# Kernel optimization log

Measured on AMD Instinct MI355X. Metric: run time of the kernel, lower is better.

The kernel has to match this reference:

```python
import jax, jax.numpy as jnp
import numpy as np

N, F_IN, D_OUT, H = 8192, 512, 64, 8
ALPHA = 0.2
NEG_INF = jnp.float32(-9e15)


def setup_inputs() -> dict:
    key = jax.random.key(0)
    k1, k2, k3, k4, k5 = jax.random.split(key, 5)
    x = jax.random.normal(k1, (N, F_IN), dtype=jnp.float32)
    # sparse-ish binary adjacency (avg degree ~33) with self-loops, stored dense
    adj = (jax.random.uniform(k2, (N, N)) < 0.004).astype(jnp.float32)
    adj = jnp.maximum(adj, jnp.eye(N, dtype=jnp.float32))
    W = jax.random.normal(k3, (H, F_IN, D_OUT), dtype=jnp.float32) * 0.05
    a1 = jax.random.normal(k4, (H, D_OUT), dtype=jnp.float32) * 0.05
    a2 = jax.random.normal(k5, (H, D_OUT), dtype=jnp.float32) * 0.05
    return {"x": x, "adj": adj, "W": W, "a1": a1, "a2": a2}


def reference(x, adj, W, a1, a2):
    mask = adj > 0
    outputs = []
    for h in range(H):  # fixed small head count (matches original per-head loop)
        Wh = x @ W[h]                      # [N, D]
        f1 = Wh @ a1[h]                    # [N]
        f2 = Wh @ a2[h]                    # [N]
        e = jax.nn.leaky_relu(f1[:, None] + f2[None, :], ALPHA)  # [N, N]
        att = jnp.where(mask, e, NEG_INF)
        att = jax.nn.softmax(att, axis=1)  # dropout omitted (eval mode)
        outputs.append(att @ Wh)           # [N, D]
    return jnp.concatenate(outputs, axis=1)  # [N, H*D]
```

## Files before the change

kernel.cpp:

```cpp
#include <hip/hip_runtime.h>
#include <hip/hip_bf16.h>
#include <cstdint>

#define N_NODES 8192
#define F_IN    512
#define D_O     64
#define H_N     8
#define NOUT    512
#define MAXD    128

#define BM 64
#define BN 128
#define BK 64

typedef __attribute__((ext_vector_type(8))) short short8;
typedef __attribute__((ext_vector_type(4))) float f32x4;

static __device__ __forceinline__ ushort f2bf(float f) {
  union { float f; uint32_t u; } v; v.f = f;
  uint32_t r = v.u + 0x7FFFu + ((v.u >> 16) & 1u);
  return (ushort)(r >> 16);
}
static __device__ __forceinline__ float bf2f(ushort u) {
  union { uint32_t u; float f; } v; v.u = ((uint32_t)u) << 16;
  return v.f;
}

__global__ __launch_bounds__(256) void convert(const float* __restrict__ x,
                                               const float* __restrict__ W,
                                               ushort* __restrict__ xb,
                                               ushort* __restrict__ Wt) {
  __shared__ float Ws[64][65];
  const int b = blockIdx.x, t = threadIdx.x;
  if (b < 2048) {
    const int gid = b * 256 + t;
    #pragma unroll
    for (int it = 0; it < 2; ++it) {
      const int q = gid + it * 524288;
      const float4 v = ((const float4*)x)[q];
      ushort4 u;
      u.x = f2bf(v.x); u.y = f2bf(v.y); u.z = f2bf(v.z); u.w = f2bf(v.w);
      ((ushort4*)xb)[q] = u;
    }
  } else {
    const int bb = b - 2048;
    const int h = bb >> 3, kt = bb & 7;
    const int d = t & 63, krg = (t >> 6) * 16;
    const float* src = &W[((size_t)h * F_IN + kt * 64 + krg) * D_O + d];
    #pragma unroll
    for (int q = 0; q < 16; ++q)
      Ws[krg + q][d] = src[(size_t)q * D_O];
    __syncthreads();
    const int d0 = t >> 2, kq = (t & 3) * 16;
    ushort* dst = &Wt[(size_t)h * D_O * F_IN + (size_t)d0 * F_IN + kt * 64 + kq];
    #pragma unroll
    for (int q = 0; q < 16; ++q)
      dst[q] = f2bf(Ws[kq + q][d0]);
  }
}

__global__ __launch_bounds__(256) void scan_gemm(const uint32_t* __restrict__ adj,
                                                 const ushort* __restrict__ xb,
                                                 const ushort* __restrict__ Wt,
                                                 const float* __restrict__ a1,
                                                 const float* __restrict__ a2,
                                                 ushort* __restrict__ Whb,
                                                 float* __restrict__ f1,
                                                 float* __restrict__ f2,
                                                 ushort* __restrict__ nbr_g,
                                                 int* __restrict__ deg_g) {
  __shared__ ushort As[BM][BK + 8];
  __shared__ ushort Bs[BN][BK + 8];
  __shared__ int wsum[4];

  const int id   = blockIdx.x;
  const int tid  = threadIdx.x;
  const int lane = tid & 63;
  const int wv   = tid >> 6;

  if (id < 512) {
    const int wr = wv >> 1, wc = wv & 1;
    const int r0 = (id >> 2) * BM;
    const int c0 = (id & 3) * BN;
    const int lm = lane & 15;
    const int lg = lane >> 4;

    f32x4 acc[2][4];
    #pragma unroll
    for (int m2 = 0; m2 < 2; ++m2)
      #pragma unroll
      for (int n2 = 0; n2 < 4; ++n2)
        acc[m2][n2] = (f32x4){0.f, 0.f, 0.f, 0.f};

    for (int k0 = 0; k0 < F_IN; k0 += BK) {
      __syncthreads();
      #pragma unroll
      for (int p = 0; p < 2; ++p) {
        const int e = p * 256 + tid;
        const int row = e >> 3, ck = (e & 7) * 8;
        *(short8*)&As[row][ck] = *(const short8*)&xb[(size_t)(r0 + row) * F_IN + k0 + ck];
      }
      #pragma unroll
      for (int p = 0; p < 4; ++p) {
        const int e = p * 256 + tid;
        const int row = e >> 3, ck = (e & 7) * 8;
        *(short8*)&Bs[row][ck] = *(const short8*)&Wt[(size_t)(c0 + row) * F_IN + k0 + ck];
      }
      __syncthreads();

      #pragma unroll
      for (int kk = 0; kk < 2; ++kk) {
        const int koff = kk * 32 + lg * 8;
        short8 af[2], bf[4];
        #pragma unroll
        for (int m2 = 0; m2 < 2; ++m2)
          af[m2] = *(const short8*)&As[wr * 32 + m2 * 16 + lm][koff];
        #pragma unroll
        for (int n2 = 0; n2 < 4; ++n2)
          bf[n2] = *(const short8*)&Bs[wc * 64 + n2 * 16 + lm][koff];
        #pragma unroll
        for (int m2 = 0; m2 < 2; ++m2)
          #pragma unroll
          for (int n2 = 0; n2 < 4; ++n2)
            acc[m2][n2] = __builtin_amdgcn_mfma_f32_16x16x32_bf16(af[m2], bf[n2], acc[m2][n2], 0, 0, 0);
      }
    }

    const int head = (c0 >> 6) + wc;
    float a1v[4], a2v[4];
    #pragma unroll
    for (int n2 = 0; n2 < 4; ++n2) {
      a1v[n2] = a1[head * D_O + n2 * 16 + lm];
      a2v[n2] = a2[head * D_O + n2 * 16 + lm];
    }
    #pragma unroll
    for (int m2 = 0; m2 < 2; ++m2) {
      #pragma unroll
      for (int r = 0; r < 4; ++r) {
        const int row = r0 + wr * 32 + m2 * 16 + lg * 4 + r;
        float p1 = 0.f, p2 = 0.f;
        #pragma unroll
        for (int n2 = 0; n2 < 4; ++n2) {
          const float v = acc[m2][n2][r];
          p1 += v * a1v[n2];
          p2 += v * a2v[n2];
          Whb[(size_t)row * NOUT + c0 + wc * 64 + n2 * 16 + lm] = f2bf(v);
        }
        #pragma unroll
        for (int o = 1; o < 16; o <<= 1) {
          p1 += __shfl_xor(p1, o);
          p2 += __shfl_xor(p2, o);
        }
        if (lm == 0) {
          f1[(size_t)row * H_N + head] = p1;
          f2[(size_t)row * H_N + head] = p2;
        }
      }
    }
  } else {
    const int i = id - 512;
    const uint32_t* arow = adj + (size_t)i * N_NODES;
    uint32_t bits = 0;
    #pragma unroll
    for (int u = 0; u < 8; ++u) {
      const uint4 a = *(const uint4*)&arow[(u * 256 + tid) * 4];
      if (a.x) bits |= 1u << (u * 4 + 0);
      if (a.y) bits |= 1u << (u * 4 + 1);
      if (a.z) bits |= 1u << (u * 4 + 2);
      if (a.w) bits |= 1u << (u * 4 + 3);
    }
    const int cnt = __popc(bits);
    int v = cnt;
    #pragma unroll
    for (int o = 1; o < 64; o <<= 1) {
      int u = __shfl_up(v, o);
      if (lane >= o) v += u;
    }
    if (lane == 63) wsum[wv] = v;
    __syncthreads();
    int base = 0, total = 0;
    #pragma unroll
    for (int ww = 0; ww < 4; ++ww) {
      int s = wsum[ww];
      if (ww < wv) base += s;
      total += s;
    }
    int off = base + v - cnt;
    #pragma unroll
    for (int u = 0; u < 8; ++u)
      #pragma unroll
      for (int bq = 0; bq < 4; ++bq)
        if (bits & (1u << (u * 4 + bq))) {
          if (off < MAXD) nbr_g[(size_t)i * MAXD + off] = (ushort)((u * 256 + tid) * 4 + bq);
          ++off;
        }
    if (tid == 0) deg_g[i] = min(total, MAXD);
  }
}

__global__ __launch_bounds__(64) void gat_panel(const ushort* __restrict__ nbr_g,
                                                const int* __restrict__ deg_g,
                                                const ushort* __restrict__ Whb,
                                                const float* __restrict__ f1,
                                                const float* __restrict__ f2,
                                                float* __restrict__ out) {
  const int bid = blockIdx.x;
  const int xcd = bid & 7;
  const int P   = xcd >> 1;
  const int i   = (bid >> 3) * 2 + (xcd & 1);
  const int t   = threadIdx.x;

  __shared__ int   nbr[MAXD];
  __shared__ float ff[MAXD][2];
  __shared__ float ps[MAXD][2];
  __shared__ float f1s2[2], invs2[2];

  const int deg = deg_g[i];
  nbr[t]      = nbr_g[(size_t)i * MAXD + t];
  nbr[t + 64] = nbr_g[(size_t)i * MAXD + t + 64];
  if (t < 2) f1s2[t] = f1[(size_t)i * H_N + 2 * P + t];
  __syncthreads();

  for (int n = t; n < deg; n += 64) {
    const float2 v = *(const float2*)&f2[(size_t)nbr[n] * H_N + 2 * P];
    ff[n][0] = v.x; ff[n][1] = v.y;
  }
  __syncthreads();

  {
    const int h = t >> 5;
    const int l = t & 31;
    const float f1v = f1s2[h];
    float m = -3.0e38f;
    for (int n = l; n < deg; n += 32) {
      float e = f1v + ff[n][h];
      e = e > 0.f ? e : 0.2f * e;
      ps[n][h] = e;
      m = fmaxf(m, e);
    }
    #pragma unroll
    for (int o = 16; o; o >>= 1) m = fmaxf(m, __shfl_xor(m, o));
    float s = 0.f;
    for (int n = l; n < deg; n += 32) {
      const float e = __expf(ps[n][h] - m);
      ps[n][h] = e;
      s += e;
    }
    #pragma unroll
    for (int o = 16; o; o >>= 1) s += __shfl_xor(s, o);
    if (l == 0) invs2[h] = 1.0f / s;
  }
  __syncthreads();

  const int ht      = t >> 5;
  const int colbase = P * 128 + t * 2;
  float a0 = 0.f, a1c = 0.f;
  #pragma unroll 8
  for (int n = 0; n < deg; ++n) {
    const float pv = ps[n][ht];
    const ushort2 u = *(const ushort2*)&Whb[(size_t)nbr[n] * NOUT + colbase];
    a0  += pv * bf2f(u.x);
    a1c += pv * bf2f(u.y);
  }
  const float inv = invs2[ht];
  float2 o2; o2.x = a0 * inv; o2.y = a1c * inv;
  *(float2*)&out[(size_t)i * NOUT + colbase] = o2;
}

extern "C" void kernel_launch(void* const* d_in, const int* in_sizes, int n_in,
                              void* d_out, int out_size, void* d_ws, size_t ws_size,
                              hipStream_t stream) {
  const float* x   = (const float*)d_in[0];
  const float* adj = (const float*)d_in[1];
  const float* W   = (const float*)d_in[2];
  const float* a1  = (const float*)d_in[3];
  const float* a2  = (const float*)d_in[4];
  float* out = (float*)d_out;

  ushort* Whb = (ushort*)d_ws;
  ushort* xb  = Whb + (size_t)N_NODES * NOUT;
  ushort* Wt  = xb + (size_t)N_NODES * F_IN;
  float*  f1  = (float*)(Wt + (size_t)H_N * D_O * F_IN);
  float*  f2  = f1 + (size_t)N_NODES * H_N;
  ushort* nbr_g = (ushort*)(f2 + (size_t)N_NODES * H_N);
  int*    deg_g = (int*)(nbr_g + (size_t)N_NODES * MAXD);

  hipLaunchKernelGGL(convert, dim3(2112), dim3(256), 0, stream, x, W, xb, Wt);
  hipLaunchKernelGGL(scan_gemm, dim3(512 + N_NODES), dim3(256), 0, stream,
                     (const uint32_t*)adj, xb, Wt, a1, a2, Whb, f1, f2, nbr_g, deg_g);
  hipLaunchKernelGGL(gat_panel, dim3(4 * N_NODES), dim3(64), 0, stream,
                     nbr_g, deg_g, Whb, f1, f2, out);
}
```

Before: 92.26 us.

## Pack four rows per block in gat_panel and drop block barriers

```diff
diff --git a/kernel.cpp b/kernel.cpp
--- a/kernel.cpp
+++ b/kernel.cpp
@@ -198,71 +198,51 @@
   }
 }
 
-__global__ __launch_bounds__(64) void gat_panel(const ushort* __restrict__ nbr_g,
-                                                const int* __restrict__ deg_g,
-                                                const ushort* __restrict__ Whb,
-                                                const float* __restrict__ f1,
-                                                const float* __restrict__ f2,
-                                                float* __restrict__ out) {
+__global__ __launch_bounds__(256) void gat_panel(const ushort* __restrict__ nbr_g,
+                                                 const int* __restrict__ deg_g,
+                                                 const ushort* __restrict__ Whb,
+                                                 const float* __restrict__ f1,
+                                                 const float* __restrict__ f2,
+                                                 float* __restrict__ out) {
   const int bid = blockIdx.x;
   const int xcd = bid & 7;
   const int P   = xcd >> 1;
-  const int i   = (bid >> 3) * 2 + (xcd & 1);
-  const int t   = threadIdx.x;
-
-  __shared__ int   nbr[MAXD];
-  __shared__ float ff[MAXD][2];
-  __shared__ float ps[MAXD][2];
-  __shared__ float f1s2[2], invs2[2];
+  const int w   = threadIdx.x >> 6;
+  const int i   = (bid >> 3) * 8 + (xcd & 1) * 4 + w;
+  const int t   = threadIdx.x & 63;
+
+  __shared__ int   nbr[4][MAXD];
+  __shared__ float ps[4][MAXD][2];
 
   const int deg = deg_g[i];
-  nbr[t]      = nbr_g[(size_t)i * MAXD + t];
-  nbr[t + 64] = nbr_g[(size_t)i * MAXD + t + 64];
-  if (t < 2) f1s2[t] = f1[(size_t)i * H_N + 2 * P + t];
-  __syncthreads();
-
-  for (int n = t; n < deg; n += 64) {
-    const float2 v = *(const float2*)&f2[(size_t)nbr[n] * H_N + 2 * P];
-    ff[n][0] = v.x; ff[n][1] = v.y;
-  }
-  __syncthreads();
-
-  {
-    const int h = t >> 5;
-    const int l = t & 31;
-    const float f1v = f1s2[h];
-    float m = -3.0e38f;
-    for (int n = l; n < deg; n += 32) {
-      float e = f1v + ff[n][h];
-      e = e > 0.f ? e : 0.2f * e;
-      ps[n][h] = e;
-      m = fmaxf(m, e);
-    }
-    #pragma unroll
-    for (int o = 16; o; o >>= 1) m = fmaxf(m, __shfl_xor(m, o));
-    float s = 0.f;
-    for (int n = l; n < deg; n += 32) {
-      const float e = __expf(ps[n][h] - m);
-      ps[n][h] = e;
-      s += e;
-    }
-    #pragma unroll
-    for (int o = 16; o; o >>= 1) s += __shfl_xor(s, o);
-    if (l == 0) invs2[h] = 1.0f / s;
-  }
-  __syncthreads();
-
-  const int ht      = t >> 5;
+  if (t < deg)      nbr[w][t]      = nbr_g[(size_t)i * MAXD + t];
+  if (t + 64 < deg) nbr[w][t + 64] = nbr_g[(size_t)i * MAXD + t + 64];
+
+  const int h = t >> 5;
+  const int l = t & 31;
+  const float f1v = f1[(size_t)i * H_N + 2 * P + h];
+  float s = 0.f;
+  for (int n = l; n < deg; n += 32) {
+    const float2 v = *(const float2*)&f2[(size_t)nbr[w][n] * H_N + 2 * P];
+    float e = f1v + (h ? v.y : v.x);
+    e = e > 0.f ? e : 0.2f * e;
+    e = __expf(e);
+    ps[w][n][h] = e;
+    s += e;
+  }
+  #pragma unroll
+  for (int o = 16; o; o >>= 1) s += __shfl_xor(s, o);
+  const float inv = 1.0f / s;
+
   const int colbase = P * 128 + t * 2;
   float a0 = 0.f, a1c = 0.f;
   #pragma unroll 8
   for (int n = 0; n < deg; ++n) {
-    const float pv = ps[n][ht];
-    const ushort2 u = *(const ushort2*)&Whb[(size_t)nbr[n] * NOUT + colbase];
+    const float pv = ps[w][n][h];
+    const ushort2 u = *(const ushort2*)&Whb[(size_t)nbr[w][n] * NOUT + colbase];
     a0  += pv * bf2f(u.x);
     a1c += pv * bf2f(u.y);
   }
-  const float inv = invs2[ht];
   float2 o2; o2.x = a0 * inv; o2.y = a1c * inv;
   *(float2*)&out[(size_t)i * NOUT + colbase] = o2;
 }
@@ -288,6 +268,6 @@
   hipLaunchKernelGGL(convert, dim3(2112), dim3(256), 0, stream, x, W, xb, Wt);
   hipLaunchKernelGGL(scan_gemm, dim3(512 + N_NODES), dim3(256), 0, stream,
                      (const uint32_t*)adj, xb, Wt, a1, a2, Whb, f1, f2, nbr_g, deg_g);
-  hipLaunchKernelGGL(gat_panel, dim3(4 * N_NODES), dim3(64), 0, stream,
+  hipLaunchKernelGGL(gat_panel, dim3(N_NODES), dim3(256), 0, stream,
                      nbr_g, deg_g, Whb, f1, f2, out);
 }
```

New measurement: 92.40 us. Within noise of the previous version (+0.1%).
